# Kernel optimization log

Hardware: AMD Instinct MI355X
Metric: run time of the kernel (lower is better)

The kernel has to match this reference:

```python
import jax, jax.numpy as jnp
import numpy as np

N_POINTS = 65536      # total nodes across the batch
NDIMS = 3
NUM_THETAS = 64       # directions
BUMP_STEPS = 32       # discretization steps of [-radius, radius]
NUM_GRAPHS = 64       # number of point clouds in the batch
RADIUS = 1.1
SCALE = 100.0         # sigmoid sharpness


def setup_inputs() -> dict:
    key = jax.random.key(0)
    k1, k2, k3 = jax.random.split(key, 3)
    x = jax.random.normal(k1, (N_POINTS, NDIMS), dtype=jnp.float32)
    # unit-norm direction vectors on the sphere, columns of v: [ndims, num_thetas]
    v = jax.random.normal(k2, (NDIMS, NUM_THETAS), dtype=jnp.float32)
    v = v / jnp.linalg.norm(v, axis=0, keepdims=True)
    # lin = discretization of [-radius, radius], matches nn.Parameter linspace
    lin = jnp.linspace(-RADIUS, RADIUS, BUMP_STEPS, dtype=jnp.float32)
    # sorted batch index assigning each node to a graph (torch_geometric convention)
    batch = jnp.sort(jax.random.randint(k3, (N_POINTS,), 0, NUM_GRAPHS, dtype=jnp.int32))
    return {"x": x, "v": v, "lin": lin, "batch": batch}


def reference(x, v, lin, batch):
    # node heights: inner product of coordinates with each direction -> [N, T]
    nh = x @ v
    # broadcast soft-threshold: sigmoid(scale * (lin - nh)) -> [N, S, T]
    # (torch builds [S,1,N,T] then movedims to [N,1,S,T]; same values)
    ecc = jax.nn.sigmoid(SCALE * (lin[None, :, None] - nh[:, None, :]))
    # segment scatter-add over nodes per graph -> [B, S, T]
    ect = jax.ops.segment_sum(ecc, batch, num_segments=NUM_GRAPHS)
    return ect  # torch output after .squeeze(): [batch, bump_steps, num_thetas]
```

## Files before the change

### kernel.cpp

```cpp
#include <hip/hip_runtime.h>

#define T      64
#define S      32
#define NGRAPH 64
#define NSPLIT 16
#define NW     4
#define TRASH  32
#define XCAP   170

__global__ __launch_bounds__(256, 4) void ect_partial(
    const float* __restrict__ x, const float* __restrict__ v,
    const float* __restrict__ lin, const int* __restrict__ batch,
    float* __restrict__ ws, int n_points)
{
    __shared__ float bins[33 * 256];
    __shared__ float x_lds[512];

    const int tid  = threadIdx.x;
    const int t    = tid & 63;
    const int w    = __builtin_amdgcn_readfirstlane(tid >> 6);
    const int b    = blockIdx.x;
    const int g    = b >> 4;
    const int c    = b & (NSPLIT - 1);

    {
        const float4 z4 = {0.0f, 0.0f, 0.0f, 0.0f};
        float4* b4 = (float4*)bins;
        for (int i = tid; i < 33 * 256 / 4; i += 256) b4[i] = z4;
    }

    const int target = (t < 32) ? g : (g + 1);
    const int i32    = t & 31;
    int lo = 0;
    const int strides[3] = {2048, 64, 2};
#pragma unroll
    for (int rnd = 0; rnd < 3; rnd++) {
        const int stride = strides[rnd];
        const int idx  = lo + i32 * stride;
        const int pv   = batch[min(idx, n_points - 1)];
        const bool prd = (idx < n_points) && (pv < target);
        const unsigned long long bal = __ballot(prd);
        const int cnt = __popc((unsigned)(bal >> (t & 32)));
        lo += max(cnt - 1, 0) * stride;
    }
    if ((lo < n_points) && (batch[min(lo, n_points - 1)] < target)) lo++;
    const int gstart = __builtin_amdgcn_readfirstlane(lo);
    const int gend   = __builtin_amdgcn_readlane(lo, 32);
    const int len    = gend - gstart;
    const int n0     = gstart + (len * c) / NSPLIT;
    const int n1     = gstart + (len * (c + 1)) / NSPLIT;
    const int sliceLen = n1 - n0;

    {
        const int base3 = 3 * n0;
        const int limit = 3 * min(sliceLen, XCAP);
        for (int p = tid; p < limit; p += 256)
            x_lds[p] = x[base3 + p];
    }

    const float lin0     = lin[0];
    const float step     = lin[1] - lin0;
    const float inv_step = 1.0f / step;
    const float nl0i     = -lin0 * inv_step;
    const float K2 = (100.0f * step) * 1.4426950408889634f;
    const float r  = __builtin_amdgcn_exp2f(-K2);

    const float v0 = v[0 * T + t];
    const float v1 = v[1 * T + t];
    const float v2 = v[2 * T + t];

    float v0acc = 0.0f;
    __syncthreads();

#define ECT_BODY(X0, X1, X2)                                                  \
    {                                                                         \
        const float nh = fmaf((X0), v0, fmaf((X1), v1, (X2) * v2));           \
        const float f  = fmaf(nh, inv_step, nl0i);                            \
        const float fs = ceilf(f);                                            \
        const int   ss = (int)fs;                                             \
        const float e0 = __builtin_amdgcn_exp2f(fmaf(K2, f - fs, K2));        \
        const float e1 = e0 * r;                                              \
        const float sm  = __builtin_amdgcn_rcpf(1.0f + e0);                   \
        const float s0v = __builtin_amdgcn_rcpf(1.0f + e1);                   \
        v0acc += (ss <= -1) ? 1.0f : (ss == 0 ? s0v : (ss == 1 ? sm : 0.0f)); \
        const int p0 = ss - 1, p1 = ss, p2 = ss + 1;                          \
        const int a0 = (((unsigned)(p0 - 1) < 31u) ? p0 : TRASH) * 256 + tid; \
        const int a1 = (((unsigned)(p1 - 1) < 31u) ? p1 : TRASH) * 256 + tid; \
        const int a2 = (((unsigned)(p2 - 1) < 31u) ? p2 : TRASH) * 256 + tid; \
        const float r0 = bins[a0], r1 = bins[a1], r2 = bins[a2];              \
        bins[a0] = r0 + sm;                                                   \
        bins[a1] = r1 + (s0v - sm);                                           \
        bins[a2] = r2 + (1.0f - s0v);                                         \
    }

    if (sliceLen <= XCAP) {
#pragma unroll 4
        for (int n = n0 + w; n < n1; n += NW) {
            const int li3 = 3 * (n - n0);
            const float x0 = x_lds[li3 + 0];
            const float x1 = x_lds[li3 + 1];
            const float x2 = x_lds[li3 + 2];
            ECT_BODY(x0, x1, x2)
        }
    } else {
#pragma unroll 2
        for (int n = n0 + w; n < n1; n += NW) {
            const float x0 = x[3 * n + 0];
            const float x1 = x[3 * n + 1];
            const float x2 = x[3 * n + 2];
            ECT_BODY(x0, x1, x2)
        }
    }
#undef ECT_BODY

    bins[0 * 256 + tid] = v0acc;
    __syncthreads();

    for (int cell = tid; cell < 32 * 64; cell += 256) {
        const int cc = cell >> 6;
        const int tt = cell & 63;
        const float sum = bins[cc * 256 +   0 + tt] + bins[cc * 256 +  64 + tt]
                        + bins[cc * 256 + 128 + tt] + bins[cc * 256 + 192 + tt];
        bins[cc * 256 + tt] = sum;
    }
    __syncthreads();

    float run = bins[0 * 256 + t];
    const int sbase = 8 * w;
    for (int cc = 1; cc < sbase; cc++) run += bins[cc * 256 + t];
    float* wsb = ws + (size_t)b * (S * T);
#pragma unroll
    for (int j = 0; j < 8; j++) {
        const int s = sbase + j;
        if (s >= 1) run += bins[s * 256 + t];
        wsb[s * T + t] = run;
    }
}

__global__ __launch_bounds__(256) void ect_reduce(
    const float4* __restrict__ ws4, float4* __restrict__ out4)
{
    const int idx = blockIdx.x * 256 + threadIdx.x;
    const int g   = idx >> 9;
    const int i   = idx & 511;
    float4 sum = {0.0f, 0.0f, 0.0f, 0.0f};
#pragma unroll
    for (int c = 0; c < NSPLIT; c++) {
        const float4 a = ws4[(size_t)(g * NSPLIT + c) * 512 + i];
        sum.x += a.x; sum.y += a.y; sum.z += a.z; sum.w += a.w;
    }
    out4[idx] = sum;
}

extern "C" void kernel_launch(void* const* d_in, const int* in_sizes, int n_in,
                              void* d_out, int out_size, void* d_ws, size_t ws_size,
                              hipStream_t stream) {
    const float* x     = (const float*)d_in[0];
    const float* v     = (const float*)d_in[1];
    const float* lin   = (const float*)d_in[2];
    const int*   batch = (const int*)d_in[3];
    float* out = (float*)d_out;
    float* ws  = (float*)d_ws;

    const int n_points = in_sizes[0] / 3;

    ect_partial<<<NGRAPH * NSPLIT, 256, 0, stream>>>(x, v, lin, batch, ws, n_points);
    ect_reduce<<<NGRAPH * S * T / 4 / 256, 256, 0, stream>>>(
        (const float4*)ws, (float4*)out);
}
```

Measured before the change: 71.68 us.

## Replace workspace reduce kernel with atomic accumulation and compact LDS bin layout

Drops the second reduction kernel and the workspace. Each split block now atomically adds its cumulative bins straight into a zeroed output, with the zeroing done by a memset on the same stream. The per-wave LDS bins are reorganised so pairs of waves share a 32x128 array, and each point updates a contiguous 3-row window whose start is clamped, which removes the trash row. Points are staged in LDS as padded float4 entries and read with one vector load each. The trade is global atomic contention (16 blocks per graph writing the same cells) plus an extra memset launch, in exchange for removing the workspace round trip and the reduce launch.

```diff
diff --git a/kernel.cpp b/kernel.cpp
--- a/kernel.cpp
+++ b/kernel.cpp
@@ -5,28 +5,31 @@
 #define NGRAPH 64
 #define NSPLIT 16
 #define NW     4
-#define TRASH  32
-#define XCAP   170
+#define XCAP   128
 
 __global__ __launch_bounds__(256, 4) void ect_partial(
     const float* __restrict__ x, const float* __restrict__ v,
     const float* __restrict__ lin, const int* __restrict__ batch,
-    float* __restrict__ ws, int n_points)
+    float* __restrict__ out, int n_points)
 {
-    __shared__ float bins[33 * 256];
-    __shared__ float x_lds[512];
+    __shared__ float bins[2][32][128];
+    __shared__ float x4[XCAP * 4];
 
     const int tid  = threadIdx.x;
     const int t    = tid & 63;
     const int w    = __builtin_amdgcn_readfirstlane(tid >> 6);
+    const int half = w >> 1;
+    const int col  = ((w & 1) << 6) + t;
+    float* bw = &bins[half][0][0];
     const int b    = blockIdx.x;
     const int g    = b >> 4;
     const int c    = b & (NSPLIT - 1);
 
     {
         const float4 z4 = {0.0f, 0.0f, 0.0f, 0.0f};
-        float4* b4 = (float4*)bins;
-        for (int i = tid; i < 33 * 256 / 4; i += 256) b4[i] = z4;
+        float4* b4 = (float4*)&bins[0][0][0];
+#pragma unroll
+        for (int i = 0; i < 8; i++) b4[tid + i * 256] = z4;
     }
 
     const int target = (t < 32) ? g : (g + 1);
@@ -52,10 +55,13 @@
     const int sliceLen = n1 - n0;
 
     {
+        const int limit = 3 * min(sliceLen, XCAP);
         const int base3 = 3 * n0;
-        const int limit = 3 * min(sliceLen, XCAP);
-        for (int p = tid; p < limit; p += 256)
-            x_lds[p] = x[base3 + p];
+        for (int p = tid; p < limit; p += 256) {
+            const int n = p / 3;
+            const int d = p - 3 * n;
+            x4[n * 4 + d] = x[base3 + p];
+        }
     }
 
     const float lin0     = lin[0];
@@ -83,24 +89,29 @@
         const float sm  = __builtin_amdgcn_rcpf(1.0f + e0);                   \
         const float s0v = __builtin_amdgcn_rcpf(1.0f + e1);                   \
         v0acc += (ss <= -1) ? 1.0f : (ss == 0 ? s0v : (ss == 1 ? sm : 0.0f)); \
-        const int p0 = ss - 1, p1 = ss, p2 = ss + 1;                          \
-        const int a0 = (((unsigned)(p0 - 1) < 31u) ? p0 : TRASH) * 256 + tid; \
-        const int a1 = (((unsigned)(p1 - 1) < 31u) ? p1 : TRASH) * 256 + tid; \
-        const int a2 = (((unsigned)(p2 - 1) < 31u) ? p2 : TRASH) * 256 + tid; \
-        const float r0 = bins[a0], r1 = bins[a1], r2 = bins[a2];              \
-        bins[a0] = r0 + sm;                                                   \
-        bins[a1] = r1 + (s0v - sm);                                           \
-        bins[a2] = r2 + (1.0f - s0v);                                         \
+        const float d1 = s0v - sm, d2 = 1.0f - s0v;                           \
+        const int pb = min(max(ss - 1, 0), 29);               \
+         \
+         \
+        const float amt0 = (pb     == ss - 1) ? sm : 0.0f;                    \
+        const float amt1 = (pb + 1 == ss    ) ? d1                            \
+                         : (pb + 1 == ss + 1) ? d2                            \
+                         : (pb + 1 == ss - 1) ? sm : 0.0f;                    \
+        const float amt2 = (pb + 2 == ss + 1) ? d2                            \
+                         : (pb + 2 == ss    ) ? d1                            \
+                         : (pb + 2 == ss - 1) ? sm : 0.0f;                    \
+        const int a = pb * 128 + col;                                         \
+        const float r0 = bw[a], r1 = bw[a + 128], r2 = bw[a + 256];           \
+        bw[a]       = r0 + amt0;                                              \
+        bw[a + 128] = r1 + amt1;                                              \
+        bw[a + 256] = r2 + amt2;                                              \
     }
 
     if (sliceLen <= XCAP) {
 #pragma unroll 4
-        for (int n = n0 + w; n < n1; n += NW) {
-            const int li3 = 3 * (n - n0);
-            const float x0 = x_lds[li3 + 0];
-            const float x1 = x_lds[li3 + 1];
-            const float x2 = x_lds[li3 + 2];
-            ECT_BODY(x0, x1, x2)
+        for (int n = w; n < sliceLen; n += NW) {
+            const float4 xv = *(const float4*)&x4[n * 4];
+            ECT_BODY(xv.x, xv.y, xv.z)
         }
     } else {
 #pragma unroll 2
@@ -113,43 +124,28 @@
     }
 #undef ECT_BODY
 
-    bins[0 * 256 + tid] = v0acc;
+    bw[col] = v0acc;
     __syncthreads();
 
     for (int cell = tid; cell < 32 * 64; cell += 256) {
         const int cc = cell >> 6;
         const int tt = cell & 63;
-        const float sum = bins[cc * 256 +   0 + tt] + bins[cc * 256 +  64 + tt]
-                        + bins[cc * 256 + 128 + tt] + bins[cc * 256 + 192 + tt];
-        bins[cc * 256 + tt] = sum;
+        const float sum = bins[0][cc][tt] + bins[0][cc][64 + tt]
+                        + bins[1][cc][tt] + bins[1][cc][64 + tt];
+        bins[0][cc][tt] = sum;
     }
     __syncthreads();
 
-    float run = bins[0 * 256 + t];
+    float run = bins[0][0][t];
     const int sbase = 8 * w;
-    for (int cc = 1; cc < sbase; cc++) run += bins[cc * 256 + t];
-    float* wsb = ws + (size_t)b * (S * T);
+    for (int cc = 1; cc < sbase; cc++) run += bins[0][cc][t];
+    float* outg = out + (size_t)g * (S * T);
 #pragma unroll
     for (int j = 0; j < 8; j++) {
         const int s = sbase + j;
-        if (s >= 1) run += bins[s * 256 + t];
-        wsb[s * T + t] = run;
+        if (s >= 1) run += bins[0][s][t];
+        atomicAdd(&outg[s * T + t], run);
     }
-}
-
-__global__ __launch_bounds__(256) void ect_reduce(
-    const float4* __restrict__ ws4, float4* __restrict__ out4)
-{
-    const int idx = blockIdx.x * 256 + threadIdx.x;
-    const int g   = idx >> 9;
-    const int i   = idx & 511;
-    float4 sum = {0.0f, 0.0f, 0.0f, 0.0f};
-#pragma unroll
-    for (int c = 0; c < NSPLIT; c++) {
-        const float4 a = ws4[(size_t)(g * NSPLIT + c) * 512 + i];
-        sum.x += a.x; sum.y += a.y; sum.z += a.z; sum.w += a.w;
-    }
-    out4[idx] = sum;
 }
 
 extern "C" void kernel_launch(void* const* d_in, const int* in_sizes, int n_in,
@@ -160,11 +156,10 @@
     const float* lin   = (const float*)d_in[2];
     const int*   batch = (const int*)d_in[3];
     float* out = (float*)d_out;
-    float* ws  = (float*)d_ws;
+    (void)d_ws; (void)ws_size;
 
     const int n_points = in_sizes[0] / 3;
 
-    ect_partial<<<NGRAPH * NSPLIT, 256, 0, stream>>>(x, v, lin, batch, ws, n_points);
-    ect_reduce<<<NGRAPH * S * T / 4 / 256, 256, 0, stream>>>(
-        (const float4*)ws, (float4*)out);
+    hipMemsetAsync(d_out, 0, out_size, stream);
+    ect_partial<<<NGRAPH * NSPLIT, 256, 0, stream>>>(x, v, lin, batch, out, n_points);
 }
```

Measured after the change: 71.93 us. No clear change (+0.3%).
